# Optimization experiments

Hardware: AMD Instinct MI355X
Metric: run time of the kernel (lower is better)

The kernel has to match this reference:

```python
import jax, jax.numpy as jnp
import numpy as np

N = 768      # n_proto (number of class prototypes)
D = 128      # trans_feat_num
H = D // 16  # edge-MLP hidden = 8
A = 312      # semantic attribute dim
INIT_TEMP = 0.1
VTEMP = 10.0
STEMP = 10.0
EPS = 1e-8


def _layer_norm(x, g, b, eps=1e-5):
    m = x.mean(-1, keepdims=True)
    v = ((x - m) ** 2).mean(-1, keepdims=True)
    return (x - m) / jnp.sqrt(v + eps) * g + b


def _instance_norm_rows(x, eps=1e-5):
    # torch InstanceNorm1d on 2D input: unbatched (C, L) -> normalize each row, no affine
    m = x.mean(-1, keepdims=True)
    v = ((x - m) ** 2).mean(-1, keepdims=True)
    return (x - m) / jnp.sqrt(v + eps)


def _init_edge(x, temp):
    # pairwise cosine similarity + row softmax
    nrm = jnp.linalg.norm(x, axis=1)
    sim = (x @ x.T) / jnp.maximum(nrm[:, None] * nrm[None, :], EPS)
    return jax.nn.softmax(sim / temp, axis=-1)


def _edge_update(proto, last_edge, W1, b1, W2, b2, temp):
    n, d = proto.shape
    # O(n^2) pairwise squared differences  -> [n*n, d]
    feat = ((proto[:, None, :] - proto[None, :, :]) ** 2).reshape(n * n, d)
    h = jax.nn.relu(_instance_norm_rows(feat @ W1.T + b1))  # [n*n, H]
    e = jnp.tanh(h @ W2.T + b2).reshape(n, n)
    return jax.nn.softmax(e * (last_edge + EPS) / temp, axis=-1)


def _node_update(proto, last_edge, edge, W, b, g, beta):
    extra = last_edge @ proto          # cross-modal message (dist_injection)
    p = edge @ proto                   # same-modal aggregation
    return jax.nn.relu(_layer_norm((p + extra) @ W.T + b, g, beta)) + p


def setup_inputs() -> dict:
    key = jax.random.key(0)
    ks = jax.random.split(key, 9)
    rn = lambda k, shape, s=1.0: jax.random.normal(k, shape, dtype=jnp.float32) * s
    return {
        "visual_proto": rn(ks[0], (N, D)),
        "semantic_proto": rn(ks[1], (N, D)),
        "attribute": rn(ks[2], (N, A)),
        "Wvn": rn(ks[3], (D, D), 0.08), "bvn": jnp.zeros((D,), jnp.float32),
        "gvn": jnp.ones((D,), jnp.float32), "betavn": jnp.zeros((D,), jnp.float32),
        "Wve1": rn(ks[4], (H, D), 0.1), "bve1": jnp.zeros((H,), jnp.float32),
        "Wve2": rn(ks[5], (1, H), 0.3), "bve2": jnp.zeros((1,), jnp.float32),
        "Wsn": rn(ks[6], (D, D), 0.08), "bsn": jnp.zeros((D,), jnp.float32),
        "gsn": jnp.ones((D,), jnp.float32), "betasn": jnp.zeros((D,), jnp.float32),
        "Wse1": rn(ks[7], (H, D), 0.1), "bse1": jnp.zeros((H,), jnp.float32),
        "Wse2": rn(ks[8], (1, H), 0.3), "bse2": jnp.zeros((1,), jnp.float32),
    }


def reference(visual_proto, semantic_proto, attribute,
              Wvn, bvn, gvn, betavn, Wve1, bve1, Wve2, bve2,
              Wsn, bsn, gsn, betasn, Wse1, bse1, Wse2, bse2):
    ve = _init_edge(visual_proto, INIT_TEMP)
    se = _init_edge(attribute, INIT_TEMP)
    vp = _node_update(visual_proto, se, ve, Wvn, bvn, gvn, betavn)
    ve2 = _edge_update(vp, ve, Wve1, bve1, Wve2, bve2, VTEMP)
    sp = _node_update(semantic_proto, ve2, se, Wsn, bsn, gsn, betasn)
    se2 = _edge_update(sp, se, Wse1, bse1, Wse2, bse2, STEMP)
    return vp, sp, ve2, se2
```

## Files before the change

kernel.cpp:

```cpp
#include <hip/hip_runtime.h>
#include <math.h>

#define NN 768
#define DD 128
#define AA 312
#define HH 8
#define CEPS 1e-8f

typedef __attribute__((ext_vector_type(8))) short s8b;
typedef __attribute__((ext_vector_type(4))) float f4v;

__device__ __forceinline__ float wave_sum(float v) {
    #pragma unroll
    for (int o = 32; o; o >>= 1) v += __shfl_down(v, o, 64);
    return v;
}
__device__ __forceinline__ float wave_max(float v) {
    #pragma unroll
    for (int o = 32; o; o >>= 1) v = fmaxf(v, __shfl_down(v, o, 64));
    return v;
}
__device__ __forceinline__ unsigned short f2bf(float f) {
    unsigned u = __float_as_uint(f);
    u += 0x7FFFu + ((u >> 16) & 1u);
    return (unsigned short)(u >> 16);
}

template <int COLS>
__device__ void gram_tile(const float* __restrict__ A, float invtemp, float* __restrict__ sim,
                          int i0, int j0, int tid, float* As, float* Bs) {
    const int tx = tid & 15, ty = tid >> 4;
    const int lr = tid >> 3, lc4 = (tid & 7) * 4;
    float acc00 = 0.f, acc01 = 0.f, acc10 = 0.f, acc11 = 0.f;
    float si0 = 0.f, si1 = 0.f, sj0 = 0.f, sj1 = 0.f;
    for (int kc = 0; kc < COLS; kc += 32) {
        float4 av, bv;
        if (kc + lc4 + 4 <= COLS) {
            av = *(const float4*)(A + (size_t)(i0 + lr) * COLS + kc + lc4);
            bv = *(const float4*)(A + (size_t)(j0 + lr) * COLS + kc + lc4);
        } else {
            float ta[4], tb[4];
            #pragma unroll
            for (int l = 0; l < 4; ++l) {
                int c = kc + lc4 + l;
                ta[l] = (c < COLS) ? A[(size_t)(i0 + lr) * COLS + c] : 0.f;
                tb[l] = (c < COLS) ? A[(size_t)(j0 + lr) * COLS + c] : 0.f;
            }
            av = make_float4(ta[0], ta[1], ta[2], ta[3]);
            bv = make_float4(tb[0], tb[1], tb[2], tb[3]);
        }
        __syncthreads();
        As[(lc4 + 0) * 34 + lr] = av.x; As[(lc4 + 1) * 34 + lr] = av.y;
        As[(lc4 + 2) * 34 + lr] = av.z; As[(lc4 + 3) * 34 + lr] = av.w;
        Bs[(lc4 + 0) * 34 + lr] = bv.x; Bs[(lc4 + 1) * 34 + lr] = bv.y;
        Bs[(lc4 + 2) * 34 + lr] = bv.z; Bs[(lc4 + 3) * 34 + lr] = bv.w;
        __syncthreads();
        #pragma unroll
        for (int k = 0; k < 32; ++k) {
            float2 aa = *(const float2*)&As[k * 34 + 2 * ty];
            float2 bb = *(const float2*)&Bs[k * 34 + 2 * tx];
            acc00 = fmaf(aa.x, bb.x, acc00);
            acc01 = fmaf(aa.x, bb.y, acc01);
            acc10 = fmaf(aa.y, bb.x, acc10);
            acc11 = fmaf(aa.y, bb.y, acc11);
            si0 = fmaf(aa.x, aa.x, si0);
            si1 = fmaf(aa.y, aa.y, si1);
            sj0 = fmaf(bb.x, bb.x, sj0);
            sj1 = fmaf(bb.y, bb.y, sj1);
        }
    }
    const float ni0 = sqrtf(si0), ni1 = sqrtf(si1);
    const float nj0 = sqrtf(sj0), nj1 = sqrtf(sj1);
    float* s0 = sim + (size_t)(i0 + 2 * ty) * NN + j0 + 2 * tx;
    float* s1 = s0 + NN;
    s0[0] = acc00 / fmaxf(ni0 * nj0, CEPS) * invtemp;
    s0[1] = acc01 / fmaxf(ni0 * nj1, CEPS) * invtemp;
    s1[0] = acc10 / fmaxf(ni1 * nj0, CEPS) * invtemp;
    s1[1] = acc11 / fmaxf(ni1 * nj1, CEPS) * invtemp;
}

__global__ __launch_bounds__(256) void gram_prep_kernel(
    const float* __restrict__ visual, const float* __restrict__ attribute,
    const float* __restrict__ Wvn, const float* __restrict__ Wsn, float* __restrict__ simv,
    float* __restrict__ sima, float* __restrict__ WvnT, float* __restrict__ WsnT) {
    __shared__ __align__(16) float smem[2176];
    const int tid = threadIdx.x;
    const int task = blockIdx.x;
    if (task < 576) {
        gram_tile<DD>(visual, 10.f, simv, (task / 24) * 32, (task % 24) * 32, tid, smem,
                      smem + 1088);
    } else if (task < 1152) {
        const int rem = task - 576;
        gram_tile<AA>(attribute, 10.f, sima, (rem / 24) * 32, (rem % 24) * 32, tid, smem,
                      smem + 1088);
    } else {
        const int u = task - 1152;
        const float* S = (u >= 16) ? Wsn : Wvn;
        float* Dt = (u >= 16) ? WsnT : WvnT;
        const int tile = u & 15;
        const int c0 = (tile & 3) * 32, r0 = (tile >> 2) * 32;
        const int tx = tid & 31, ty = tid >> 5;
        #pragma unroll
        for (int rr = ty; rr < 32; rr += 8)
            smem[rr * 33 + tx] = S[(size_t)(r0 + rr) * DD + c0 + tx];
        __syncthreads();
        #pragma unroll
        for (int rr = ty; rr < 32; rr += 8)
            Dt[(size_t)(c0 + rr) * DD + r0 + tx] = smem[tx * 33 + rr];
    }
}

__device__ void block_softmax768(float* buf, int tid, float* red) {
    const int w = tid >> 6, lane = tid & 63;
    float v0 = buf[tid];
    float v1 = (tid < NN - 512) ? buf[tid + 512] : -3.4e38f;
    float m = wave_max(fmaxf(v0, v1));
    if (lane == 0) red[w] = m;
    __syncthreads();
    m = red[0];
    #pragma unroll
    for (int i = 1; i < 8; ++i) m = fmaxf(m, red[i]);
    float e0 = __expf(v0 - m);
    float e1 = (tid < NN - 512) ? __expf(v1 - m) : 0.f;
    float sw = wave_sum(e0 + e1);
    if (lane == 0) red[8 + w] = sw;
    __syncthreads();
    float s = 0.f;
    #pragma unroll
    for (int i = 0; i < 8; ++i) s += red[8 + i];
    const float inv = 1.f / s;
    buf[tid] = e0 * inv;
    if (tid < NN - 512) buf[tid + 512] = e1 * inv;
    __syncthreads();
}

template <bool SMEP, bool SMEX>
__global__ __launch_bounds__(512) void node_kernel(
    const float* __restrict__ P, const float* __restrict__ EpSrc, const float* __restrict__ ExSrc,
    const float* __restrict__ WT, const float* __restrict__ b, const float* __restrict__ g,
    const float* __restrict__ beta, float* __restrict__ out, const float* __restrict__ W1e,
    short* __restrict__ outb, float* __restrict__ cvec) {
    __shared__ __align__(16) float ep[2][NN], ex[2][NN];
    __shared__ __align__(16) float pp[4][2][DD], xx[4][2][DD];
    __shared__ __align__(16) float qs[2][DD], tps[2][2][DD];
    __shared__ float red[16];
    const int i0 = blockIdx.x * 2;
    const int tid = threadIdx.x;
    const int s = (tid >> 7) & 3, d = tid & 127;
    if (tid < 384) {
        ((float4*)ep)[tid] = ((const float4*)(EpSrc + (size_t)i0 * NN))[tid];
        ((float4*)ex)[tid] = ((const float4*)(ExSrc + (size_t)i0 * NN))[tid];
    }
    __syncthreads();
    if (SMEP) {
        block_softmax768(ep[0], tid, red);
        block_softmax768(ep[1], tid, red);
    }
    if (SMEX) {
        block_softmax768(ex[0], tid, red);
        block_softmax768(ex[1], tid, red);
    }
    float p0 = 0.f, x0 = 0.f, p1 = 0.f, x1 = 0.f;
    const int kb = s * 192;
    #pragma unroll 4
    for (int kk = 0; kk < 192; ++kk) {
        const int k = kb + kk;
        const float pv = P[(size_t)k * DD + d];
        p0 = fmaf(ep[0][k], pv, p0);
        x0 = fmaf(ex[0][k], pv, x0);
        p1 = fmaf(ep[1][k], pv, p1);
        x1 = fmaf(ex[1][k], pv, x1);
    }
    pp[s][0][d] = p0; xx[s][0][d] = x0;
    pp[s][1][d] = p1; xx[s][1][d] = x1;
    __syncthreads();
    const int rr = (tid >> 7) & 1;
    float preg = 0.f;
    if (tid < 256) {
        float p = pp[0][rr][d] + pp[1][rr][d] + pp[2][rr][d] + pp[3][rr][d];
        float x = xx[0][rr][d] + xx[1][rr][d] + xx[2][rr][d] + xx[3][rr][d];
        qs[rr][d] = p + x;
        preg = p;
    }
    __syncthreads();
    {
        const int sc = tid >> 8, rr2 = (tid >> 7) & 1;
        float t = (sc == 0) ? b[d] : 0.f;
        const int c0 = sc * 64;
        #pragma unroll 4
        for (int c = c0; c < c0 + 64; ++c) t = fmaf(qs[rr2][c], WT[(size_t)c * DD + d], t);
        tps[sc][rr2][d] = t;
    }
    __syncthreads();
    float tval = 0.f;
    if (tid < 256) tval = tps[0][rr][d] + tps[1][rr][d];
    float sm = wave_sum(tid < 256 ? tval : 0.f);
    if ((tid & 63) == 0) red[tid >> 6] = sm;
    __syncthreads();
    if (tid < 256) tval -= (red[2 * rr] + red[2 * rr + 1]) * (1.f / DD);
    float s2 = wave_sum(tid < 256 ? tval * tval : 0.f);
    if ((tid & 63) == 0) red[8 + (tid >> 6)] = s2;
    __syncthreads();
    if (tid < 256) {
        const float var = (red[8 + 2 * rr] + red[8 + 2 * rr + 1]) * (1.f / DD);
        const float ln = tval * rsqrtf(var + 1e-5f) * g[d] + beta[d];
        const float val = fmaxf(ln, 0.f) + preg;
        out[(size_t)(i0 + rr) * DD + d] = val;
        outb[(size_t)(i0 + rr) * DD + d] = (short)f2bf(val);
        qs[rr][d] = val;
    }
    __syncthreads();
    if (tid < 256) {
        const int row = tid >> 7, r = (tid >> 4) & 7, l16 = tid & 15;
        float ssum = 0.f;
        #pragma unroll
        for (int t = 0; t < 8; ++t) {
            const int k = l16 + 16 * t;
            const float pv = qs[row][k];
            ssum = fmaf(W1e[r * DD + k], pv * pv, ssum);
        }
        #pragma unroll
        for (int o = 8; o; o >>= 1) ssum += __shfl_down(ssum, o, 16);
        if (l16 == 0) cvec[(size_t)(i0 + row) * HH + r] = ssum;
    }
}

__global__ __launch_bounds__(512) void edge_fused_kernel(
    const float* __restrict__ PR, const short* __restrict__ PRb, const float* __restrict__ cvec,
    const float* __restrict__ ELraw, const float* __restrict__ W1, const float* __restrict__ b1,
    const float* __restrict__ W2, const float* __restrict__ b2, float invtemp,
    float* __restrict__ out) {
    const int i0 = blockIdx.x * 2;
    const int tid = threadIdx.x;
    const int lane = tid & 63, wave = tid >> 6;
    __shared__ __align__(16) float pi[2][DD];
    __shared__ __align__(16) float w1s[HH * DD];
    __shared__ __align__(16) short a_sw[4 * 64 * 8];
    __shared__ __align__(16) float Ls[2][NN];
    __shared__ __align__(16) float Els[2][NN];
    __shared__ float red[16];
    if (tid < 256) {
        pi[tid >> 7][tid & 127] = PR[(size_t)(i0 + (tid >> 7)) * DD + (tid & 127)];
        ((float4*)w1s)[tid] = ((const float4*)W1)[tid];
    }
    if (tid < 384)
        ((float4*)Els)[tid] = ((const float4*)(ELraw + (size_t)i0 * NN))[tid];
    __syncthreads();
    block_softmax768(Els[0], tid, red);
    block_softmax768(Els[1], tid, red);
    if (tid < 256) {
        const int t = tid >> 6, m = lane & 15, q2 = lane >> 4;
        const int il = m >> 3, r = m & 7;
        const int kb = t * 32 + q2 * 8;
        s8b av;
        #pragma unroll
        for (int e = 0; e < 8; ++e)
            av[e] = (short)f2bf(pi[il][kb + e] * w1s[r * DD + kb + e]);
        *(s8b*)&a_sw[(t * 64 + lane) * 8] = av;
    }
    __syncthreads();
    s8b af[4];
    #pragma unroll
    for (int t = 0; t < 4; ++t) af[t] = *(const s8b*)&a_sw[(t * 64 + lane) * 8];
    const int q = lane >> 4, n = lane & 15;
    const int rbase = (q & 1) * 4;
    const int il = q >> 1;
    const float4 ci4 = *(const float4*)&cvec[(size_t)(i0 + il) * HH + rbase];
    const float4 b14 = *(const float4*)&b1[rbase];
    const float4 w24 = *(const float4*)&W2[rbase];
    const float b2s = b2[0];
    #pragma unroll
    for (int s = 0; s < 6; ++s) {
        const int j = wave * 96 + s * 16 + n;
        f4v acc = {0.f, 0.f, 0.f, 0.f};
        #pragma unroll
        for (int t = 0; t < 4; ++t) {
            const s8b bf = *(const s8b*)(PRb + (size_t)j * DD + t * 32 + q * 8);
            acc = __builtin_amdgcn_mfma_f32_16x16x32_bf16(af[t], bf, acc, 0, 0, 0);
        }
        const float4 cj = *(const float4*)&cvec[(size_t)j * HH + rbase];
        float z[4];
        z[0] = ci4.x + cj.x - 2.f * acc[0] + b14.x;
        z[1] = ci4.y + cj.y - 2.f * acc[1] + b14.y;
        z[2] = ci4.z + cj.z - 2.f * acc[2] + b14.z;
        z[3] = ci4.w + cj.w - 2.f * acc[3] + b14.w;
        float s1 = z[0] + z[1] + z[2] + z[3];
        float s2 = z[0] * z[0] + z[1] * z[1] + z[2] * z[2] + z[3] * z[3];
        s1 += __shfl_xor(s1, 16, 64);
        s2 += __shfl_xor(s2, 16, 64);
        const float mean = s1 * (1.f / HH);
        const float var = fmaxf(s2 * (1.f / HH) - mean * mean, 0.f);
        const float istd = rsqrtf(var + 1e-5f);
        float a2 = 0.f;
        a2 = fmaf(fmaxf((z[0] - mean) * istd, 0.f), w24.x, a2);
        a2 = fmaf(fmaxf((z[1] - mean) * istd, 0.f), w24.y, a2);
        a2 = fmaf(fmaxf((z[2] - mean) * istd, 0.f), w24.z, a2);
        a2 = fmaf(fmaxf((z[3] - mean) * istd, 0.f), w24.w, a2);
        a2 += __shfl_xor(a2, 16, 64);
        const float tv = tanhf(a2 + b2s);
        const float lv = Els[il][j];
        if ((q & 1) == 0) Ls[il][j] = tv * (lv + CEPS) * invtemp;
    }
    __syncthreads();
    block_softmax768(Ls[0], tid, red);
    block_softmax768(Ls[1], tid, red);
    float* d0 = out + (size_t)i0 * NN;
    float* d1 = out + (size_t)(i0 + 1) * NN;
    d0[tid] = Ls[0][tid];
    d1[tid] = Ls[1][tid];
    if (tid < NN - 512) {
        d0[tid + 512] = Ls[0][tid + 512];
        d1[tid + 512] = Ls[1][tid + 512];
    }
}

extern "C" void kernel_launch(void* const* d_in, const int* in_sizes, int n_in, void* d_out,
                              int out_size, void* d_ws, size_t ws_size, hipStream_t stream) {
    const float* visual    = (const float*)d_in[0];
    const float* semantic  = (const float*)d_in[1];
    const float* attribute = (const float*)d_in[2];
    const float* Wvn  = (const float*)d_in[3];
    const float* bvn  = (const float*)d_in[4];
    const float* gvn  = (const float*)d_in[5];
    const float* betavn = (const float*)d_in[6];
    const float* Wve1 = (const float*)d_in[7];
    const float* bve1 = (const float*)d_in[8];
    const float* Wve2 = (const float*)d_in[9];
    const float* bve2 = (const float*)d_in[10];
    const float* Wsn  = (const float*)d_in[11];
    const float* bsn  = (const float*)d_in[12];
    const float* gsn  = (const float*)d_in[13];
    const float* betasn = (const float*)d_in[14];
    const float* Wse1 = (const float*)d_in[15];
    const float* bse1 = (const float*)d_in[16];
    const float* Wse2 = (const float*)d_in[17];
    const float* bse2 = (const float*)d_in[18];

    float* out = (float*)d_out;
    float* vp  = out;
    float* sp  = out + 98304;
    float* ve2 = out + 196608;
    float* se2 = out + 786432;

    float* ws    = (float*)d_ws;
    float* simv  = ws;
    float* sima  = ws + 589824;
    float* WvnT  = ws + 2949120;
    float* WsnT  = ws + 2965504;
    float* cvec1 = ws + 2981888;
    float* cvec2 = ws + 2988032;
    short* vpb   = (short*)(ws + 2994176);
    short* spb   = (short*)(ws + 3043328);

    gram_prep_kernel<<<1184, 256, 0, stream>>>(visual, attribute, Wvn, Wsn, simv, sima, WvnT,
                                               WsnT);
    node_kernel<true, true><<<NN / 2, 512, 0, stream>>>(visual, simv, sima, WvnT, bvn, gvn,
                                                        betavn, vp, Wve1, vpb, cvec1);
    edge_fused_kernel<<<NN / 2, 512, 0, stream>>>(vp, vpb, cvec1, simv, Wve1, bve1, Wve2, bve2,
                                                  0.1f, ve2);
    node_kernel<true, false><<<NN / 2, 512, 0, stream>>>(semantic, sima, ve2, WsnT, bsn, gsn,
                                                         betasn, sp, Wse1, spb, cvec2);
    edge_fused_kernel<<<NN / 2, 512, 0, stream>>>(sp, spb, cvec2, sima, Wse1, bse1, Wse2, bse2,
                                                  0.1f, se2);
}
```

Before: 197.6 us.

## Fuse all five stages into one cooperative persistent kernel with grid syncs

Replaces the five separate kernel launches with a single cooperative kernel that loops over tasks for each stage, separated by grid-wide barriers. Shared memory is carved manually from one buffer, and the gram stage runs two 256-thread tasks per 512-thread block. This removes launch gaps and inter-kernel drain between dependent stages. In exchange it adds grid.sync costs, caps the grid at 512 blocks so each stage's work is spread across persistent blocks, and falls back to the old multi-launch path if the cooperative launch fails.

```diff
diff --git a/kernel.cpp b/kernel.cpp
--- a/kernel.cpp
+++ b/kernel.cpp
@@ -1,11 +1,15 @@
 #include <hip/hip_runtime.h>
+#include <hip/hip_cooperative_groups.h>
 #include <math.h>
+
+namespace cg = cooperative_groups;
 
 #define NN 768
 #define DD 128
 #define AA 312
 #define HH 8
 #define CEPS 1e-8f
+#define SMEM_F 5920
 
 typedef __attribute__((ext_vector_type(8))) short s8b;
 typedef __attribute__((ext_vector_type(4))) float f4v;
@@ -25,6 +29,15 @@
     u += 0x7FFFu + ((u >> 16) & 1u);
     return (unsigned short)(u >> 16);
 }
+
+struct KParams {
+    const float *visual, *semantic, *attribute;
+    const float *Wvn, *bvn, *gvn, *betavn, *Wve1, *bve1, *Wve2, *bve2;
+    const float *Wsn, *bsn, *gsn, *betasn, *Wse1, *bse1, *Wse2, *bse2;
+    float *vp, *sp, *ve2, *se2;
+    float *simv, *sima, *WvnT, *WsnT, *cvec1, *cvec2;
+    short *vpb, *spb;
+};
 
 template <int COLS>
 __device__ void gram_tile(const float* __restrict__ A, float invtemp, float* __restrict__ sim,
@@ -79,34 +92,28 @@
     s1[1] = acc11 / fmaxf(ni1 * nj1, CEPS) * invtemp;
 }
 
-__global__ __launch_bounds__(256) void gram_prep_kernel(
-    const float* __restrict__ visual, const float* __restrict__ attribute,
-    const float* __restrict__ Wvn, const float* __restrict__ Wsn, float* __restrict__ simv,
-    float* __restrict__ sima, float* __restrict__ WvnT, float* __restrict__ WsnT) {
-    __shared__ __align__(16) float smem[2176];
-    const int tid = threadIdx.x;
-    const int task = blockIdx.x;
+__device__ void gram_task(const KParams& p, int task, int st, float* my) {
     if (task < 576) {
-        gram_tile<DD>(visual, 10.f, simv, (task / 24) * 32, (task % 24) * 32, tid, smem,
-                      smem + 1088);
+        gram_tile<DD>(p.visual, 10.f, p.simv, (task / 24) * 32, (task % 24) * 32, st, my,
+                      my + 1088);
     } else if (task < 1152) {
         const int rem = task - 576;
-        gram_tile<AA>(attribute, 10.f, sima, (rem / 24) * 32, (rem % 24) * 32, tid, smem,
-                      smem + 1088);
+        gram_tile<AA>(p.attribute, 10.f, p.sima, (rem / 24) * 32, (rem % 24) * 32, st, my,
+                      my + 1088);
     } else {
         const int u = task - 1152;
-        const float* S = (u >= 16) ? Wsn : Wvn;
-        float* Dt = (u >= 16) ? WsnT : WvnT;
+        const float* S = (u >= 16) ? p.Wsn : p.Wvn;
+        float* Dt = (u >= 16) ? p.WsnT : p.WvnT;
         const int tile = u & 15;
         const int c0 = (tile & 3) * 32, r0 = (tile >> 2) * 32;
-        const int tx = tid & 31, ty = tid >> 5;
+        const int tx = st & 31, ty = st >> 5;
         #pragma unroll
         for (int rr = ty; rr < 32; rr += 8)
-            smem[rr * 33 + tx] = S[(size_t)(r0 + rr) * DD + c0 + tx];
+            my[rr * 33 + tx] = S[(size_t)(r0 + rr) * DD + c0 + tx];
         __syncthreads();
         #pragma unroll
         for (int rr = ty; rr < 32; rr += 8)
-            Dt[(size_t)(c0 + rr) * DD + r0 + tx] = smem[tx * 33 + rr];
+            Dt[(size_t)(c0 + rr) * DD + r0 + tx] = my[tx * 33 + rr];
     }
 }
 
@@ -135,17 +142,20 @@
 }
 
 template <bool SMEP, bool SMEX>
-__global__ __launch_bounds__(512) void node_kernel(
-    const float* __restrict__ P, const float* __restrict__ EpSrc, const float* __restrict__ ExSrc,
-    const float* __restrict__ WT, const float* __restrict__ b, const float* __restrict__ g,
-    const float* __restrict__ beta, float* __restrict__ out, const float* __restrict__ W1e,
-    short* __restrict__ outb, float* __restrict__ cvec) {
-    __shared__ __align__(16) float ep[2][NN], ex[2][NN];
-    __shared__ __align__(16) float pp[4][2][DD], xx[4][2][DD];
-    __shared__ __align__(16) float qs[2][DD], tps[2][2][DD];
-    __shared__ float red[16];
-    const int i0 = blockIdx.x * 2;
-    const int tid = threadIdx.x;
+__device__ void node_body(const float* __restrict__ P, const float* __restrict__ EpSrc,
+                          const float* __restrict__ ExSrc, const float* __restrict__ WT,
+                          const float* __restrict__ b, const float* __restrict__ g,
+                          const float* __restrict__ beta, float* __restrict__ out,
+                          const float* __restrict__ W1e, short* __restrict__ outb,
+                          float* __restrict__ cvec, int bid, int tid, float* smem) {
+    float (*ep)[NN] = (float (*)[NN])smem;
+    float (*ex)[NN] = (float (*)[NN])(smem + 2 * NN);
+    float (*pp)[2][DD] = (float (*)[2][DD])(smem + 4 * NN);
+    float (*xx)[2][DD] = (float (*)[2][DD])(smem + 4 * NN + 1024);
+    float (*qs)[DD] = (float (*)[DD])(smem + 4 * NN + 2048);
+    float (*tps)[2][DD] = (float (*)[2][DD])(smem + 4 * NN + 2304);
+    float* red = smem + 4 * NN + 2816;
+    const int i0 = bid * 2;
     const int s = (tid >> 7) & 3, d = tid & 127;
     if (tid < 384) {
         ((float4*)ep)[tid] = ((const float4*)(EpSrc + (size_t)i0 * NN))[tid];
@@ -223,22 +233,22 @@
         for (int o = 8; o; o >>= 1) ssum += __shfl_down(ssum, o, 16);
         if (l16 == 0) cvec[(size_t)(i0 + row) * HH + r] = ssum;
     }
-}
-
-__global__ __launch_bounds__(512) void edge_fused_kernel(
-    const float* __restrict__ PR, const short* __restrict__ PRb, const float* __restrict__ cvec,
-    const float* __restrict__ ELraw, const float* __restrict__ W1, const float* __restrict__ b1,
-    const float* __restrict__ W2, const float* __restrict__ b2, float invtemp,
-    float* __restrict__ out) {
-    const int i0 = blockIdx.x * 2;
-    const int tid = threadIdx.x;
+    __syncthreads();
+}
+
+__device__ void edge_body(const float* __restrict__ PR, const short* __restrict__ PRb,
+                          const float* __restrict__ cvec, const float* __restrict__ ELraw,
+                          const float* __restrict__ W1, const float* __restrict__ b1,
+                          const float* __restrict__ W2, const float* __restrict__ b2,
+                          float invtemp, float* __restrict__ out, int bid, int tid, float* smem) {
+    float (*pi)[DD] = (float (*)[DD])smem;
+    float* w1s = smem + 256;
+    short* a_sw = (short*)(smem + 1280);
+    float (*Ls)[NN] = (float (*)[NN])(smem + 2304);
+    float (*Els)[NN] = (float (*)[NN])(smem + 3840);
+    float* red = smem + 5376;
+    const int i0 = bid * 2;
     const int lane = tid & 63, wave = tid >> 6;
-    __shared__ __align__(16) float pi[2][DD];
-    __shared__ __align__(16) float w1s[HH * DD];
-    __shared__ __align__(16) short a_sw[4 * 64 * 8];
-    __shared__ __align__(16) float Ls[2][NN];
-    __shared__ __align__(16) float Els[2][NN];
-    __shared__ float red[16];
     if (tid < 256) {
         pi[tid >> 7][tid & 127] = PR[(size_t)(i0 + (tid >> 7)) * DD + (tid & 127)];
         ((float4*)w1s)[tid] = ((const float4*)W1)[tid];
@@ -312,54 +322,149 @@
         d0[tid + 512] = Ls[0][tid + 512];
         d1[tid + 512] = Ls[1][tid + 512];
     }
+    __syncthreads();
+}
+
+__global__ __launch_bounds__(256) void gram_prep_kernel(KParams p) {
+    __shared__ __align__(16) float smem[2176];
+    gram_task(p, blockIdx.x, threadIdx.x, smem);
+}
+template <bool SMEP, bool SMEX>
+__global__ __launch_bounds__(512) void node_kernel(const float* P, const float* EpSrc,
+                                                   const float* ExSrc, const float* WT,
+                                                   const float* b, const float* g,
+                                                   const float* beta, float* out,
+                                                   const float* W1e, short* outb, float* cvec) {
+    __shared__ __align__(16) float smem[SMEM_F];
+    node_body<SMEP, SMEX>(P, EpSrc, ExSrc, WT, b, g, beta, out, W1e, outb, cvec, blockIdx.x,
+                          threadIdx.x, smem);
+}
+__global__ __launch_bounds__(512) void edge_kernel(const float* PR, const short* PRb,
+                                                   const float* cvec, const float* ELraw,
+                                                   const float* W1, const float* b1,
+                                                   const float* W2, const float* b2,
+                                                   float invtemp, float* out) {
+    __shared__ __align__(16) float smem[SMEM_F];
+    edge_body(PR, PRb, cvec, ELraw, W1, b1, W2, b2, invtemp, out, blockIdx.x, threadIdx.x, smem);
+}
+
+__global__ __launch_bounds__(512, 4) void fused_all(KParams p) {
+    cg::grid_group grid = cg::this_grid();
+    __shared__ __align__(16) float smem[SMEM_F];
+    const int tid = threadIdx.x;
+    const int bid = blockIdx.x;
+    const int nb = gridDim.x;
+
+    {
+        const int half = tid >> 8;
+        const int st = tid & 255;
+        float* my = smem + half * 2176;
+        for (int pr = bid; pr < 592; pr += nb) {
+            gram_task(p, pr * 2 + half, st, my);
+            __syncthreads();
+        }
+    }
+    __threadfence();
+    grid.sync();
+    for (int t = bid; t < 384; t += nb)
+        node_body<true, true>(p.visual, p.simv, p.sima, p.WvnT, p.bvn, p.gvn, p.betavn, p.vp,
+                              p.Wve1, p.vpb, p.cvec1, t, tid, smem);
+    __threadfence();
+    grid.sync();
+    for (int t = bid; t < 384; t += nb)
+        edge_body(p.vp, p.vpb, p.cvec1, p.simv, p.Wve1, p.bve1, p.Wve2, p.bve2, 0.1f, p.ve2, t,
+                  tid, smem);
+    __threadfence();
+    grid.sync();
+    for (int t = bid; t < 384; t += nb)
+        node_body<true, false>(p.semantic, p.sima, p.ve2, p.WsnT, p.bsn, p.gsn, p.betasn, p.sp,
+                               p.Wse1, p.spb, p.cvec2, t, tid, smem);
+    __threadfence();
+    grid.sync();
+    for (int t = bid; t < 384; t += nb)
+        edge_body(p.sp, p.spb, p.cvec2, p.sima, p.Wse1, p.bse1, p.Wse2, p.bse2, 0.1f, p.se2, t,
+                  tid, smem);
 }
 
 extern "C" void kernel_launch(void* const* d_in, const int* in_sizes, int n_in, void* d_out,
                               int out_size, void* d_ws, size_t ws_size, hipStream_t stream) {
-    const float* visual    = (const float*)d_in[0];
-    const float* semantic  = (const float*)d_in[1];
-    const float* attribute = (const float*)d_in[2];
-    const float* Wvn  = (const float*)d_in[3];
-    const float* bvn  = (const float*)d_in[4];
-    const float* gvn  = (const float*)d_in[5];
-    const float* betavn = (const float*)d_in[6];
-    const float* Wve1 = (const float*)d_in[7];
-    const float* bve1 = (const float*)d_in[8];
-    const float* Wve2 = (const float*)d_in[9];
-    const float* bve2 = (const float*)d_in[10];
-    const float* Wsn  = (const float*)d_in[11];
-    const float* bsn  = (const float*)d_in[12];
-    const float* gsn  = (const float*)d_in[13];
-    const float* betasn = (const float*)d_in[14];
-    const float* Wse1 = (const float*)d_in[15];
-    const float* bse1 = (const float*)d_in[16];
-    const float* Wse2 = (const float*)d_in[17];
-    const float* bse2 = (const float*)d_in[18];
+    KParams kp;
+    kp.visual    = (const float*)d_in[0];
+    kp.semantic  = (const float*)d_in[1];
+    kp.attribute = (const float*)d_in[2];
+    kp.Wvn  = (const float*)d_in[3];
+    kp.bvn  = (const float*)d_in[4];
+    kp.gvn  = (const float*)d_in[5];
+    kp.betavn = (const float*)d_in[6];
+    kp.Wve1 = (const float*)d_in[7];
+    kp.bve1 = (const float*)d_in[8];
+    kp.Wve2 = (const float*)d_in[9];
+    kp.bve2 = (const float*)d_in[10];
+    kp.Wsn  = (const float*)d_in[11];
+    kp.bsn  = (const float*)d_in[12];
+    kp.gsn  = (const float*)d_in[13];
+    kp.betasn = (const float*)d_in[14];
+    kp.Wse1 = (const float*)d_in[15];
+    kp.bse1 = (const float*)d_in[16];
+    kp.Wse2 = (const float*)d_in[17];
+    kp.bse2 = (const float*)d_in[18];
 
     float* out = (float*)d_out;
-    float* vp  = out;
-    float* sp  = out + 98304;
-    float* ve2 = out + 196608;
-    float* se2 = out + 786432;
-
-    float* ws    = (float*)d_ws;
-    float* simv  = ws;
-    float* sima  = ws + 589824;
-    float* WvnT  = ws + 2949120;
-    float* WsnT  = ws + 2965504;
-    float* cvec1 = ws + 2981888;
-    float* cvec2 = ws + 2988032;
-    short* vpb   = (short*)(ws + 2994176);
-    short* spb   = (short*)(ws + 3043328);
-
-    gram_prep_kernel<<<1184, 256, 0, stream>>>(visual, attribute, Wvn, Wsn, simv, sima, WvnT,
-                                               WsnT);
-    node_kernel<true, true><<<NN / 2, 512, 0, stream>>>(visual, simv, sima, WvnT, bvn, gvn,
-                                                        betavn, vp, Wve1, vpb, cvec1);
-    edge_fused_kernel<<<NN / 2, 512, 0, stream>>>(vp, vpb, cvec1, simv, Wve1, bve1, Wve2, bve2,
-                                                  0.1f, ve2);
-    node_kernel<true, false><<<NN / 2, 512, 0, stream>>>(semantic, sima, ve2, WsnT, bsn, gsn,
-                                                         betasn, sp, Wse1, spb, cvec2);
-    edge_fused_kernel<<<NN / 2, 512, 0, stream>>>(sp, spb, cvec2, sima, Wse1, bse1, Wse2, bse2,
-                                                  0.1f, se2);
-}
+    kp.vp  = out;
+    kp.sp  = out + 98304;
+    kp.ve2 = out + 196608;
+    kp.se2 = out + 786432;
+
+    float* ws = (float*)d_ws;
+    kp.simv  = ws;
+    kp.sima  = ws + 589824;
+    kp.WvnT  = ws + 2949120;
+    kp.WsnT  = ws + 2965504;
+    kp.cvec1 = ws + 2981888;
+    kp.cvec2 = ws + 2988032;
+    kp.vpb   = (short*)(ws + 2994176);
+    kp.spb   = (short*)(ws + 3043328);
+
+    static int coop_state = 0;
+    static int coop_grid = 0;
+
+    bool did_coop = false;
+    if (coop_state >= 0) {
+        if (coop_grid == 0) {
+            int bpc = 0;
+            hipError_t qe = hipOccupancyMaxActiveBlocksPerMultiprocessor(
+                &bpc, (const void*)fused_all, 512, 0);
+            if (qe != hipSuccess || bpc < 1) {
+                coop_state = -1;
+            } else {
+                coop_grid = bpc * 256;
+                if (coop_grid > 512) coop_grid = 512;
+            }
+        }
+        if (coop_state >= 0) {
+            void* args[] = {(void*)&kp};
+            hipError_t le = hipLaunchCooperativeKernel((const void*)fused_all,
+                                                       dim3(coop_grid), dim3(512), args, 0,
+                                                       stream);
+            if (le == hipSuccess) {
+                coop_state = 1;
+                did_coop = true;
+            } else {
+                coop_state = -1;
+            }
+        }
+    }
+    if (!did_coop) {
+        gram_prep_kernel<<<1184, 256, 0, stream>>>(kp);
+        node_kernel<true, true><<<NN / 2, 512, 0, stream>>>(kp.visual, kp.simv, kp.sima,
+                                                            kp.WvnT, kp.bvn, kp.gvn, kp.betavn,
+                                                            kp.vp, kp.Wve1, kp.vpb, kp.cvec1);
+        edge_kernel<<<NN / 2, 512, 0, stream>>>(kp.vp, kp.vpb, kp.cvec1, kp.simv, kp.Wve1,
+                                                kp.bve1, kp.Wve2, kp.bve2, 0.1f, kp.ve2);
+        node_kernel<true, false><<<NN / 2, 512, 0, stream>>>(kp.semantic, kp.sima, kp.ve2,
+                                                             kp.WsnT, kp.bsn, kp.gsn, kp.betasn,
+                                                             kp.sp, kp.Wse1, kp.spb, kp.cvec2);
+        edge_kernel<<<NN / 2, 512, 0, stream>>>(kp.sp, kp.spb, kp.cvec2, kp.sima, kp.Wse1,
+                                                kp.bse1, kp.Wse2, kp.bse2, 0.1f, kp.se2);
+    }
+}
```

Measured after the change: 234.5 us. 18.7% more time.

## Compute Gram matrices with split-bf16 MFMA and defer cosine normalization

Applied to the files above, without the earlier changes.

Replaces the scalar FP32 Gram tile computation with 64x64 tiles computed on MFMA, using a hi/lo bf16 split with three products to approximate FP32 accuracy. Row norms are taken from the Gram diagonal and written to a small buffer. The cosine division and temperature scaling move into the node and edge kernels just before their softmax. This cuts ALU work in the first kernel and its block count, but adds per-row normalization passes and some loss of precision from the bf16 split.

```diff
diff --git a/kernel.cpp b/kernel.cpp
--- a/kernel.cpp
+++ b/kernel.cpp
@@ -6,6 +6,7 @@
 #define AA 312
 #define HH 8
 #define CEPS 1e-8f
+#define SMEM_F 5920
 
 typedef __attribute__((ext_vector_type(8))) short s8b;
 typedef __attribute__((ext_vector_type(4))) float f4v;
@@ -26,77 +27,91 @@
     return (unsigned short)(u >> 16);
 }
 
-template <int COLS>
-__device__ void gram_tile(const float* __restrict__ A, float invtemp, float* __restrict__ sim,
-                          int i0, int j0, int tid, float* As, float* Bs) {
-    const int tx = tid & 15, ty = tid >> 4;
-    const int lr = tid >> 3, lc4 = (tid & 7) * 4;
-    float acc00 = 0.f, acc01 = 0.f, acc10 = 0.f, acc11 = 0.f;
-    float si0 = 0.f, si1 = 0.f, sj0 = 0.f, sj1 = 0.f;
-    for (int kc = 0; kc < COLS; kc += 32) {
-        float4 av, bv;
-        if (kc + lc4 + 4 <= COLS) {
-            av = *(const float4*)(A + (size_t)(i0 + lr) * COLS + kc + lc4);
-            bv = *(const float4*)(A + (size_t)(j0 + lr) * COLS + kc + lc4);
-        } else {
-            float ta[4], tb[4];
+struct KParams {
+    const float *visual, *semantic, *attribute;
+    const float *Wvn, *bvn, *gvn, *betavn, *Wve1, *bve1, *Wve2, *bve2;
+    const float *Wsn, *bsn, *gsn, *betasn, *Wse1, *bse1, *Wse2, *bse2;
+    float *vp, *sp, *ve2, *se2;
+    float *simv, *sima, *WvnT, *WsnT, *cvec1, *cvec2;
+    float *nrmv, *nrma;
+    short *vpb, *spb;
+};
+
+__global__ __launch_bounds__(256) void gram_mfma_kernel(KParams p) {
+    __shared__ __align__(16) unsigned short AH[64 * 40];
+    __shared__ __align__(16) unsigned short AL[64 * 40];
+    __shared__ __align__(16) unsigned short BH[64 * 40];
+    __shared__ __align__(16) unsigned short BL[64 * 40];
+    const int task = blockIdx.x;
+    const int tid = threadIdx.x;
+    if (task < 288) {
+        const bool isv = (task < 144);
+        const int tt = isv ? task : task - 144;
+        const int bi = tt / 12, bj = tt % 12;
+        const float* M = isv ? p.visual : p.attribute;
+        float* G = isv ? p.simv : p.sima;
+        float* nrm = isv ? p.nrmv : p.nrma;
+        const int K = isv ? DD : AA;
+        const int i0 = bi * 64, j0 = bj * 64;
+        const int w = tid >> 6, lane = tid & 63;
+        const int m = lane & 15, q = lane >> 4;
+        f4v acc[4] = {{0.f, 0.f, 0.f, 0.f}, {0.f, 0.f, 0.f, 0.f},
+                      {0.f, 0.f, 0.f, 0.f}, {0.f, 0.f, 0.f, 0.f}};
+        const int nchunk = (K + 31) >> 5;
+        const int srow = tid >> 2, sq = (tid & 3) * 8;
+        for (int c = 0; c < nchunk; ++c) {
+            const int kc = c * 32;
+            __syncthreads();
             #pragma unroll
-            for (int l = 0; l < 4; ++l) {
-                int c = kc + lc4 + l;
-                ta[l] = (c < COLS) ? A[(size_t)(i0 + lr) * COLS + c] : 0.f;
-                tb[l] = (c < COLS) ? A[(size_t)(j0 + lr) * COLS + c] : 0.f;
+            for (int h = 0; h < 2; ++h) {
+                const int col = sq + h * 4;
+                float4 a = {0.f, 0.f, 0.f, 0.f}, b = {0.f, 0.f, 0.f, 0.f};
+                if (kc + col + 4 <= K) {
+                    a = *(const float4*)(M + (size_t)(i0 + srow) * K + kc + col);
+                    b = *(const float4*)(M + (size_t)(j0 + srow) * K + kc + col);
+                }
+                const float av[4] = {a.x, a.y, a.z, a.w};
+                const float bv[4] = {b.x, b.y, b.z, b.w};
+                #pragma unroll
+                for (int e = 0; e < 4; ++e) {
+                    const unsigned short ah = f2bf(av[e]);
+                    const float ahf = __uint_as_float((unsigned)ah << 16);
+                    const unsigned short al = f2bf(av[e] - ahf);
+                    const unsigned short bh = f2bf(bv[e]);
+                    const float bhf = __uint_as_float((unsigned)bh << 16);
+                    const unsigned short bl = f2bf(bv[e] - bhf);
+                    AH[srow * 40 + col + e] = ah;
+                    AL[srow * 40 + col + e] = al;
+                    BH[srow * 40 + col + e] = bh;
+                    BL[srow * 40 + col + e] = bl;
+                }
             }
-            av = make_float4(ta[0], ta[1], ta[2], ta[3]);
-            bv = make_float4(tb[0], tb[1], tb[2], tb[3]);
+            __syncthreads();
+            const s8b ah8 = *(const s8b*)&AH[(w * 16 + m) * 40 + q * 8];
+            const s8b al8 = *(const s8b*)&AL[(w * 16 + m) * 40 + q * 8];
+            #pragma unroll
+            for (int jt = 0; jt < 4; ++jt) {
+                const s8b bh8 = *(const s8b*)&BH[(jt * 16 + m) * 40 + q * 8];
+                const s8b bl8 = *(const s8b*)&BL[(jt * 16 + m) * 40 + q * 8];
+                acc[jt] = __builtin_amdgcn_mfma_f32_16x16x32_bf16(ah8, bh8, acc[jt], 0, 0, 0);
+                acc[jt] = __builtin_amdgcn_mfma_f32_16x16x32_bf16(ah8, bl8, acc[jt], 0, 0, 0);
+                acc[jt] = __builtin_amdgcn_mfma_f32_16x16x32_bf16(al8, bh8, acc[jt], 0, 0, 0);
+            }
         }
-        __syncthreads();
-        As[(lc4 + 0) * 34 + lr] = av.x; As[(lc4 + 1) * 34 + lr] = av.y;
-        As[(lc4 + 2) * 34 + lr] = av.z; As[(lc4 + 3) * 34 + lr] = av.w;
-        Bs[(lc4 + 0) * 34 + lr] = bv.x; Bs[(lc4 + 1) * 34 + lr] = bv.y;
-        Bs[(lc4 + 2) * 34 + lr] = bv.z; Bs[(lc4 + 3) * 34 + lr] = bv.w;
-        __syncthreads();
-        #pragma unroll
-        for (int k = 0; k < 32; ++k) {
-            float2 aa = *(const float2*)&As[k * 34 + 2 * ty];
-            float2 bb = *(const float2*)&Bs[k * 34 + 2 * tx];
-            acc00 = fmaf(aa.x, bb.x, acc00);
-            acc01 = fmaf(aa.x, bb.y, acc01);
-            acc10 = fmaf(aa.y, bb.x, acc10);
-            acc11 = fmaf(aa.y, bb.y, acc11);
-            si0 = fmaf(aa.x, aa.x, si0);
-            si1 = fmaf(aa.y, aa.y, si1);
-            sj0 = fmaf(bb.x, bb.x, sj0);
-            sj1 = fmaf(bb.y, bb.y, sj1);
+        #pragma unroll
+        for (int jt = 0; jt < 4; ++jt) {
+            #pragma unroll
+            for (int r = 0; r < 4; ++r) {
+                G[(size_t)(i0 + w * 16 + q * 4 + r) * NN + j0 + jt * 16 + m] = acc[jt][r];
+                if (bi == bj && jt == w && m == q * 4 + r)
+                    nrm[i0 + w * 16 + m] = sqrtf(fmaxf(acc[jt][r], 0.f));
+            }
         }
-    }
-    const float ni0 = sqrtf(si0), ni1 = sqrtf(si1);
-    const float nj0 = sqrtf(sj0), nj1 = sqrtf(sj1);
-    float* s0 = sim + (size_t)(i0 + 2 * ty) * NN + j0 + 2 * tx;
-    float* s1 = s0 + NN;
-    s0[0] = acc00 / fmaxf(ni0 * nj0, CEPS) * invtemp;
-    s0[1] = acc01 / fmaxf(ni0 * nj1, CEPS) * invtemp;
-    s1[0] = acc10 / fmaxf(ni1 * nj0, CEPS) * invtemp;
-    s1[1] = acc11 / fmaxf(ni1 * nj1, CEPS) * invtemp;
-}
-
-__global__ __launch_bounds__(256) void gram_prep_kernel(
-    const float* __restrict__ visual, const float* __restrict__ attribute,
-    const float* __restrict__ Wvn, const float* __restrict__ Wsn, float* __restrict__ simv,
-    float* __restrict__ sima, float* __restrict__ WvnT, float* __restrict__ WsnT) {
-    __shared__ __align__(16) float smem[2176];
-    const int tid = threadIdx.x;
-    const int task = blockIdx.x;
-    if (task < 576) {
-        gram_tile<DD>(visual, 10.f, simv, (task / 24) * 32, (task % 24) * 32, tid, smem,
-                      smem + 1088);
-    } else if (task < 1152) {
-        const int rem = task - 576;
-        gram_tile<AA>(attribute, 10.f, sima, (rem / 24) * 32, (rem % 24) * 32, tid, smem,
-                      smem + 1088);
     } else {
-        const int u = task - 1152;
-        const float* S = (u >= 16) ? Wsn : Wvn;
-        float* Dt = (u >= 16) ? WsnT : WvnT;
+        float* smem = (float*)AH;
+        const int u = task - 288;
+        const float* S = (u >= 16) ? p.Wsn : p.Wvn;
+        float* Dt = (u >= 16) ? p.WsnT : p.WvnT;
         const int tile = u & 15;
         const int c0 = (tile & 3) * 32, r0 = (tile >> 2) * 32;
         const int tx = tid & 31, ty = tid >> 5;
@@ -134,9 +149,19 @@
     __syncthreads();
 }
 
+__device__ void norm_rows(float (*buf)[NN], const float* __restrict__ nrm, int i0, int tid) {
+    const float n0 = nrm[i0], n1 = nrm[i0 + 1];
+    for (int k = tid; k < NN; k += 512) {
+        const float nj = nrm[k];
+        buf[0][k] = buf[0][k] * 10.f / fmaxf(n0 * nj, CEPS);
+        buf[1][k] = buf[1][k] * 10.f / fmaxf(n1 * nj, CEPS);
+    }
+}
+
 template <bool SMEP, bool SMEX>
 __global__ __launch_bounds__(512) void node_kernel(
     const float* __restrict__ P, const float* __restrict__ EpSrc, const float* __restrict__ ExSrc,
+    const float* __restrict__ nrmP, const float* __restrict__ nrmX,
     const float* __restrict__ WT, const float* __restrict__ b, const float* __restrict__ g,
     const float* __restrict__ beta, float* __restrict__ out, const float* __restrict__ W1e,
     short* __restrict__ outb, float* __restrict__ cvec) {
@@ -153,10 +178,12 @@
     }
     __syncthreads();
     if (SMEP) {
+        norm_rows(ep, nrmP, i0, tid);
         block_softmax768(ep[0], tid, red);
         block_softmax768(ep[1], tid, red);
     }
     if (SMEX) {
+        norm_rows(ex, nrmX, i0, tid);
         block_softmax768(ex[0], tid, red);
         block_softmax768(ex[1], tid, red);
     }
@@ -225,20 +252,20 @@
     }
 }
 
-__global__ __launch_bounds__(512) void edge_fused_kernel(
+__global__ __launch_bounds__(512) void edge_kernel(
     const float* __restrict__ PR, const short* __restrict__ PRb, const float* __restrict__ cvec,
-    const float* __restrict__ ELraw, const float* __restrict__ W1, const float* __restrict__ b1,
-    const float* __restrict__ W2, const float* __restrict__ b2, float invtemp,
-    float* __restrict__ out) {
-    const int i0 = blockIdx.x * 2;
-    const int tid = threadIdx.x;
-    const int lane = tid & 63, wave = tid >> 6;
+    const float* __restrict__ ELraw, const float* __restrict__ nrmE,
+    const float* __restrict__ W1, const float* __restrict__ b1, const float* __restrict__ W2,
+    const float* __restrict__ b2, float invtemp, float* __restrict__ out) {
     __shared__ __align__(16) float pi[2][DD];
     __shared__ __align__(16) float w1s[HH * DD];
     __shared__ __align__(16) short a_sw[4 * 64 * 8];
     __shared__ __align__(16) float Ls[2][NN];
     __shared__ __align__(16) float Els[2][NN];
     __shared__ float red[16];
+    const int i0 = blockIdx.x * 2;
+    const int tid = threadIdx.x;
+    const int lane = tid & 63, wave = tid >> 6;
     if (tid < 256) {
         pi[tid >> 7][tid & 127] = PR[(size_t)(i0 + (tid >> 7)) * DD + (tid & 127)];
         ((float4*)w1s)[tid] = ((const float4*)W1)[tid];
@@ -246,6 +273,7 @@
     if (tid < 384)
         ((float4*)Els)[tid] = ((const float4*)(ELraw + (size_t)i0 * NN))[tid];
     __syncthreads();
+    norm_rows(Els, nrmE, i0, tid);
     block_softmax768(Els[0], tid, red);
     block_softmax768(Els[1], tid, red);
     if (tid < 256) {
@@ -316,50 +344,54 @@
 
 extern "C" void kernel_launch(void* const* d_in, const int* in_sizes, int n_in, void* d_out,
                               int out_size, void* d_ws, size_t ws_size, hipStream_t stream) {
-    const float* visual    = (const float*)d_in[0];
-    const float* semantic  = (const float*)d_in[1];
-    const float* attribute = (const float*)d_in[2];
-    const float* Wvn  = (const float*)d_in[3];
-    const float* bvn  = (const float*)d_in[4];
-    const float* gvn  = (const float*)d_in[5];
-    const float* betavn = (const float*)d_in[6];
-    const float* Wve1 = (const float*)d_in[7];
-    const float* bve1 = (const float*)d_in[8];
-    const float* Wve2 = (const float*)d_in[9];
-    const float* bve2 = (const float*)d_in[10];
-    const float* Wsn  = (const float*)d_in[11];
-    const float* bsn  = (const float*)d_in[12];
-    const float* gsn  = (const float*)d_in[13];
-    const float* betasn = (const float*)d_in[14];
-    const float* Wse1 = (const float*)d_in[15];
-    const float* bse1 = (const float*)d_in[16];
-    const float* Wse2 = (const float*)d_in[17];
-    const float* bse2 = (const float*)d_in[18];
+    KParams kp;
+    kp.visual    = (const float*)d_in[0];
+    kp.semantic  = (const float*)d_in[1];
+    kp.attribute = (const float*)d_in[2];
+    kp.Wvn  = (const float*)d_in[3];
+    kp.bvn  = (const float*)d_in[4];
+    kp.gvn  = (const float*)d_in[5];
+    kp.betavn = (const float*)d_in[6];
+    kp.Wve1 = (const float*)d_in[7];
+    kp.bve1 = (const float*)d_in[8];
+    kp.Wve2 = (const float*)d_in[9];
+    kp.bve2 = (const float*)d_in[10];
+    kp.Wsn  = (const float*)d_in[11];
+    kp.bsn  = (const float*)d_in[12];
+    kp.gsn  = (const float*)d_in[13];
+    kp.betasn = (const float*)d_in[14];
+    kp.Wse1 = (const float*)d_in[15];
+    kp.bse1 = (const float*)d_in[16];
+    kp.Wse2 = (const float*)d_in[17];
+    kp.bse2 = (const float*)d_in[18];
 
     float* out = (float*)d_out;
-    float* vp  = out;
-    float* sp  = out + 98304;
-    float* ve2 = out + 196608;
-    float* se2 = out + 786432;
-
-    float* ws    = (float*)d_ws;
-    float* simv  = ws;
-    float* sima  = ws + 589824;
-    float* WvnT  = ws + 2949120;
-    float* WsnT  = ws + 2965504;
-    float* cvec1 = ws + 2981888;
-    float* cvec2 = ws + 2988032;
-    short* vpb   = (short*)(ws + 2994176);
-    short* spb   = (short*)(ws + 3043328);
-
-    gram_prep_kernel<<<1184, 256, 0, stream>>>(visual, attribute, Wvn, Wsn, simv, sima, WvnT,
-                                               WsnT);
-    node_kernel<true, true><<<NN / 2, 512, 0, stream>>>(visual, simv, sima, WvnT, bvn, gvn,
-                                                        betavn, vp, Wve1, vpb, cvec1);
-    edge_fused_kernel<<<NN / 2, 512, 0, stream>>>(vp, vpb, cvec1, simv, Wve1, bve1, Wve2, bve2,
-                                                  0.1f, ve2);
-    node_kernel<true, false><<<NN / 2, 512, 0, stream>>>(semantic, sima, ve2, WsnT, bsn, gsn,
-                                                         betasn, sp, Wse1, spb, cvec2);
-    edge_fused_kernel<<<NN / 2, 512, 0, stream>>>(sp, spb, cvec2, sima, Wse1, bse1, Wse2, bse2,
-                                                  0.1f, se2);
-}
+    kp.vp  = out;
+    kp.sp  = out + 98304;
+    kp.ve2 = out + 196608;
+    kp.se2 = out + 786432;
+
+    float* ws = (float*)d_ws;
+    kp.simv  = ws;
+    kp.sima  = ws + 589824;
+    kp.WvnT  = ws + 2949120;
+    kp.WsnT  = ws + 2965504;
+    kp.cvec1 = ws + 2981888;
+    kp.cvec2 = ws + 2988032;
+    kp.vpb   = (short*)(ws + 2994176);
+    kp.spb   = (short*)(ws + 3043328);
+    kp.nrmv  = ws + 3092480;
+    kp.nrma  = ws + 3093248;
+
+    gram_mfma_kernel<<<320, 256, 0, stream>>>(kp);
+    node_kernel<true, true><<<NN / 2, 512, 0, stream>>>(
+        kp.visual, kp.simv, kp.sima, kp.nrmv, kp.nrma, kp.WvnT, kp.bvn, kp.gvn, kp.betavn,
+        kp.vp, kp.Wve1, kp.vpb, kp.cvec1);
+    edge_kernel<<<NN / 2, 512, 0, stream>>>(kp.vp, kp.vpb, kp.cvec1, kp.simv, kp.nrmv, kp.Wve1,
+                                            kp.bve1, kp.Wve2, kp.bve2, 0.1f, kp.ve2);
+    node_kernel<true, false><<<NN / 2, 512, 0, stream>>>(
+        kp.semantic, kp.sima, kp.ve2, kp.nrma, nullptr, kp.WsnT, kp.bsn, kp.gsn, kp.betasn,
+        kp.sp, kp.Wse1, kp.spb, kp.cvec2);
+    edge_kernel<<<NN / 2, 512, 0, stream>>>(kp.sp, kp.spb, kp.cvec2, kp.sima, kp.nrma, kp.Wse1,
+                                            kp.bse1, kp.Wse2, kp.bse2, 0.1f, kp.se2);
+}
```

Result: faster. 190.4 us (-3.6%).
